# Kernel optimization log

Measured on AMD Instinct MI355X. Metric: run time of the kernel, lower is better.

Reference implementation:

```python
import jax, jax.numpy as jnp
import numpy as np

B, S, D, H = 2, 2048, 1024, 16
HD = D // H


def setup_inputs() -> dict:
    key = jax.random.key(0)
    ks = jax.random.split(key, 8)
    scale = 1.0 / np.sqrt(D)
    return {
        "x": jax.random.normal(ks[0], (B, S, D), dtype=jnp.float32),
        "y": jax.random.normal(ks[1], (B, S, D), dtype=jnp.float32),
        "gamma": jnp.ones((D,), jnp.float32),
        "beta": jnp.zeros((D,), jnp.float32),
        "in_proj_w": jax.random.uniform(ks[2], (3 * D, D), jnp.float32, -scale, scale),
        "in_proj_b": jnp.zeros((3 * D,), jnp.float32),
        "out_w": jax.random.uniform(ks[3], (D, D), jnp.float32, -scale, scale),
        "out_b": jnp.zeros((D,), jnp.float32),
    }


def _layer_norm(x, gamma, beta, eps=1e-5):
    mu = jnp.mean(x, axis=-1, keepdims=True)
    var = jnp.mean((x - mu) ** 2, axis=-1, keepdims=True)
    return (x - mu) * jax.lax.rsqrt(var + eps) * gamma + beta


def reference(x, y, gamma, beta, in_proj_w, in_proj_b, out_w, out_b):
    # Pre-LN (note: y is unused by the original forward; q=k=v=norm(x))
    xn = _layer_norm(x, gamma, beta)
    # combined QKV projection, PyTorch convention: xn @ W^T + b
    qkv = jnp.einsum("bsd,ed->bse", xn, in_proj_w) + in_proj_b  # (B,S,3D)
    q, k, v = jnp.split(qkv, 3, axis=-1)
    # (B,H,S,HD)
    q = q.reshape(B, S, H, HD).transpose(0, 2, 1, 3)
    k = k.reshape(B, S, H, HD).transpose(0, 2, 1, 3)
    v = v.reshape(B, S, H, HD).transpose(0, 2, 1, 3)
    scores = jnp.einsum("bhqd,bhkd->bhqk", q, k) / np.sqrt(HD)
    attn = jax.nn.softmax(scores, axis=-1)  # (B,H,S,S)
    ctx = jnp.einsum("bhqk,bhkd->bhqd", attn, v)
    ctx = ctx.transpose(0, 2, 1, 3).reshape(B, S, D)
    out = jnp.einsum("bsd,ed->bse", ctx, out_w) + out_b
    # dropout p=0.0 -> identity; residual
    out = out + x
    # average_attn_weights=True default in PyTorch
    attn_w = jnp.mean(attn, axis=1)  # (B,S,S)
    return out, attn_w
```

## Files before the change

### kernel.cpp

```cpp
#include <hip/hip_runtime.h>
#include <hip/hip_bf16.h>

#define Bb 2
#define Ss 2048
#define Dd 1024
#define Hh 16
#define HDd 64
#define Mm (Bb*Ss)
#define N3 (3*Dd)

typedef __attribute__((ext_vector_type(8))) __bf16 bf16x8;
typedef __attribute__((ext_vector_type(4))) float f32x4;
typedef __attribute__((ext_vector_type(16))) float f32x16;
typedef __attribute__((ext_vector_type(8))) short short8;

__device__ __forceinline__ unsigned short f2b(float f) {
  unsigned int u = __float_as_uint(f);
  return (unsigned short)((u + 0x7fffu + ((u >> 16) & 1u)) >> 16);
}

__device__ __forceinline__ f32x4 mfma16(bf16x8 a, bf16x8 b, f32x4 c) {
  return __builtin_amdgcn_mfma_f32_16x16x32_bf16(a, b, c, 0, 0, 0);
}
__device__ __forceinline__ f32x16 mfma32(bf16x8 a, bf16x8 b, f32x16 c) {
  return __builtin_amdgcn_mfma_f32_32x32x16_bf16(a, b, c, 0, 0, 0);
}
__device__ __forceinline__ unsigned cvtpk(float lo, float hi) {
  unsigned r; asm("v_cvt_pk_bf16_f32 %0, %1, %2" : "=v"(r) : "v"(lo), "v"(hi)); return r;
}
__device__ __forceinline__ float fexp2(float x) {
  float r; asm("v_exp_f32 %0, %1" : "=v"(r) : "v"(x)); return r;
}
__device__ __forceinline__ void gload16(const unsigned short* g, unsigned short* l) {
  __builtin_amdgcn_global_load_lds((const __attribute__((address_space(1))) void*)g,
                                   (__attribute__((address_space(3))) void*)l, 16, 0, 0);
}

__global__ __launch_bounds__(256) void prep_kernel(const float* __restrict__ x,
                                                   const float* __restrict__ gamma,
                                                   const float* __restrict__ beta,
                                                   unsigned short* __restrict__ xn,
                                                   const float* __restrict__ w_in,
                                                   unsigned short* __restrict__ wqkv,
                                                   const float* __restrict__ w_out,
                                                   unsigned short* __restrict__ wout) {
  const int bid = blockIdx.x, t = threadIdx.x;
  if (bid < Mm) {
    const float* xr = x + (size_t)bid * Dd;
    float4 v = ((const float4*)xr)[t];
    float s  = v.x + v.y + v.z + v.w;
    float ss = v.x*v.x + v.y*v.y + v.z*v.z + v.w*v.w;
    for (int m = 1; m < 64; m <<= 1) { s += __shfl_xor(s, m, 64); ss += __shfl_xor(ss, m, 64); }
    __shared__ float rs[4], rss[4];
    int w = t >> 6;
    if ((t & 63) == 0) { rs[w] = s; rss[w] = ss; }
    __syncthreads();
    s  = rs[0] + rs[1] + rs[2] + rs[3];
    ss = rss[0] + rss[1] + rss[2] + rss[3];
    float mu   = s * (1.0f / Dd);
    float var  = ss * (1.0f / Dd) - mu * mu;
    float rstd = rsqrtf(var + 1e-5f);
    float4 g  = ((const float4*)gamma)[t];
    float4 be = ((const float4*)beta)[t];
    ushort4 o;
    o.x = f2b((v.x - mu) * rstd * g.x + be.x);
    o.y = f2b((v.y - mu) * rstd * g.y + be.y);
    o.z = f2b((v.z - mu) * rstd * g.z + be.z);
    o.w = f2b((v.w - mu) * rstd * g.w + be.w);
    ((ushort4*)(xn + (size_t)bid * Dd))[t] = o;
  } else if (bid < Mm + 1024) {
    const int b2 = bid - Mm;
    for (int i = b2*256 + t; i < (N3*Dd)/4; i += 1024*256) {
      float4 v = ((const float4*)w_in)[i];
      ushort4 u; u.x = f2b(v.x); u.y = f2b(v.y); u.z = f2b(v.z); u.w = f2b(v.w);
      ((ushort4*)wqkv)[i] = u;
    }
  } else {
    const int b2 = bid - Mm - 1024;
    for (int i = b2*256 + t; i < (Dd*Dd)/4; i += 512*256) {
      float4 v = ((const float4*)w_out)[i];
      ushort4 u; u.x = f2b(v.x); u.y = f2b(v.y); u.z = f2b(v.z); u.w = f2b(v.w);
      ((ushort4*)wout)[i] = u;
    }
  }
}

__global__ __launch_bounds__(256) void qkv_gemm_kernel(
    const unsigned short* __restrict__ A, const unsigned short* __restrict__ Bw,
    const float* __restrict__ bias,
    unsigned short* __restrict__ qb, unsigned short* __restrict__ kb,
    unsigned short* __restrict__ vtb) {
  __shared__ __align__(16) unsigned short As[64][64];
  __shared__ __align__(16) unsigned short Bs[128][64];
  const int t = threadIdx.x, l = t & 63, w = t >> 6;
  const int wr = w >> 1, wc = w & 1;
  const int lin = blockIdx.x;
  const int swz = (lin & 7) * 192 + (lin >> 3);
  const int mb = (swz & 63) * 64, nb = (swz >> 6) * 128;
  const int sc8 = ((l & 7) ^ ((l >> 3) & 7)) * 8;
  f32x4 acc[2][4];
  for (int i = 0; i < 2; i++) for (int j = 0; j < 4; j++) acc[i][j] = f32x4{0.f,0.f,0.f,0.f};
  for (int kt = 0; kt < 1024; kt += 64) {
    __syncthreads();
#pragma unroll
    for (int j = 0; j < 2; ++j) {
      int rbase = w*16 + j*8;
      gload16(&A[(size_t)(mb + rbase + (l >> 3))*1024 + kt + sc8], &As[rbase][0]);
    }
#pragma unroll
    for (int j = 0; j < 4; ++j) {
      int rbase = w*32 + j*8;
      gload16(&Bw[(size_t)(nb + rbase + (l >> 3))*1024 + kt + sc8], &Bs[rbase][0]);
    }
    __syncthreads();
#pragma unroll
    for (int ks = 0; ks < 2; ++ks) {
      bf16x8 af[2], bfr[4];
      const int g = ks*4 + (l >> 4);
#pragma unroll
      for (int i = 0; i < 2; i++) {
        int row = wr*32 + i*16 + (l & 15);
        af[i] = *(const bf16x8*)&As[row][(g ^ (row & 7))*8];
      }
#pragma unroll
      for (int j = 0; j < 4; j++) {
        int row = wc*64 + j*16 + (l & 15);
        bfr[j] = *(const bf16x8*)&Bs[row][(g ^ (row & 7))*8];
      }
#pragma unroll
      for (int i = 0; i < 2; i++)
#pragma unroll
        for (int j = 0; j < 4; j++)
          acc[i][j] = mfma16(af[i], bfr[j], acc[i][j]);
    }
  }
  const int rbase = (l >> 4) * 4;
#pragma unroll
  for (int i = 0; i < 2; i++) {
#pragma unroll
    for (int j = 0; j < 4; j++) {
      int ncol = nb + wc*64 + j*16 + (l & 15);
      int which = ncol >> 10, d = ncol & 1023, h = d >> 6, hd = d & 63;
      float bv = bias[ncol];
      int mrow0 = mb + wr*32 + i*16 + rbase;
      int b = mrow0 >> 11, s0 = mrow0 & 2047;
      if (which == 2) {
        ushort4 u;
        u.x = f2b(acc[i][j][0] + bv); u.y = f2b(acc[i][j][1] + bv);
        u.z = f2b(acc[i][j][2] + bv); u.w = f2b(acc[i][j][3] + bv);
        *(ushort4*)&vtb[((size_t)(b*Hh + h)*HDd + hd)*Ss + s0] = u;
      } else {
        unsigned short* dst = (which == 0) ? qb : kb;
        float sc = (which == 0) ? 0.18033688f : 1.0f;
#pragma unroll
        for (int r = 0; r < 4; r++)
          dst[((size_t)(b*Hh + h)*Ss + s0 + r)*HDd + hd] = f2b((acc[i][j][r] + bv) * sc);
      }
    }
  }
}

__global__ __launch_bounds__(512) void ctx_kernel(const unsigned short* __restrict__ q,
                                                  const unsigned short* __restrict__ k,
                                                  const unsigned short* __restrict__ vt,
                                                  float* __restrict__ linv,
                                                  unsigned short* __restrict__ ctxb) {
  const int bh = blockIdx.x, qt = blockIdx.y;
  const int b = bh >> 4, h = bh & 15;
  const unsigned short* qp  = q  + (size_t)bh * Ss * HDd;
  const unsigned short* kp  = k  + (size_t)bh * Ss * HDd;
  const unsigned short* vtp = vt + (size_t)bh * HDd * Ss;
  const int t = threadIdx.x, l = t & 63, w = t >> 6;
  const int wq = w & 3, wk = w >> 2;
  const int l31 = l & 31, hi = l >> 5;
  __shared__ __align__(16) unsigned short Ks[2][2][64][64];
  __shared__ __align__(16) unsigned short Vs[2][2][64][64];
  __shared__ float ls[8][32];
  const int qbase = qt*128 + wq*32;
  const int sc8 = ((l & 7) ^ ((l >> 3) & 7)) * 8;
  const int kofs = wk * 1024;
  bf16x8 qfr[4];
#pragma unroll
  for (int c = 0; c < 4; ++c)
    qfr[c] = *(const bf16x8*)&qp[(size_t)(qbase + l31)*HDd + c*16 + hi*8];
#pragma unroll
  for (int j = 0; j < 2; ++j) {
    int rbase = wq*16 + j*8;
    int row = rbase + (l >> 3);
    gload16(&kp [(size_t)(kofs + row)*HDd + sc8], &Ks[wk][0][rbase][0]);
    gload16(&vtp[(size_t)row*Ss + kofs + sc8],    &Vs[wk][0][rbase][0]);
  }
  __syncthreads();

  f32x16 cacc[2];
#pragma unroll
  for (int dj = 0; dj < 2; ++dj)
#pragma unroll
    for (int r = 0; r < 16; ++r) cacc[dj][r] = 0.f;
  float lsum = 0.f;

  for (int it = 0; it < 16; ++it) {
    const int cur = it & 1;
    if (it < 15) {
      int kt = kofs + (it + 1) * 64;
#pragma unroll
      for (int j = 0; j < 2; ++j) {
        int rbase = wq*16 + j*8;
        int row = rbase + (l >> 3);
        gload16(&kp [(size_t)(kt + row)*HDd + sc8], &Ks[wk][cur^1][rbase][0]);
        gload16(&vtp[(size_t)row*Ss + kt + sc8],    &Vs[wk][cur^1][rbase][0]);
      }
    }
#pragma unroll
    for (int kj = 0; kj < 2; ++kj) {
      f32x16 sacc;
#pragma unroll
      for (int r = 0; r < 16; ++r) sacc[r] = 0.f;
      __builtin_amdgcn_s_setprio(1);
#pragma unroll
      for (int c = 0; c < 4; ++c) {
        int R = kj*32 + l31;
        int s = 2*c + hi;
        bf16x8 kf = *(const bf16x8*)&Ks[wk][cur][R][(s ^ (R & 7))*8];
        sacc = mfma32(kf, qfr[c], sacc);
      }
      __builtin_amdgcn_s_setprio(0);
      float p[16];
#pragma unroll
      for (int r = 0; r < 16; ++r) { p[r] = fexp2(sacc[r]); lsum += p[r]; }
      unsigned xa = cvtpk(p[0],p[1]),   xb = cvtpk(p[4],p[5]);
      unsigned ya = cvtpk(p[2],p[3]),   yb = cvtpk(p[6],p[7]);
      unsigned za = cvtpk(p[8],p[9]),   zb = cvtpk(p[12],p[13]);
      unsigned wa = cvtpk(p[10],p[11]), wb = cvtpk(p[14],p[15]);
      asm volatile("v_permlane32_swap_b32 %0, %1" : "+v"(xa), "+v"(xb));
      asm volatile("v_permlane32_swap_b32 %0, %1" : "+v"(ya), "+v"(yb));
      asm volatile("v_permlane32_swap_b32 %0, %1" : "+v"(za), "+v"(zb));
      asm volatile("v_permlane32_swap_b32 %0, %1" : "+v"(wa), "+v"(wb));
      union { unsigned u[4]; bf16x8 v; } f0, f1;
      f0.u[0]=xa; f0.u[1]=ya; f0.u[2]=xb; f0.u[3]=yb;
      f1.u[0]=za; f1.u[1]=wa; f1.u[2]=zb; f1.u[3]=wb;
      __builtin_amdgcn_s_setprio(1);
#pragma unroll
      for (int kc = 0; kc < 2; ++kc) {
        bf16x8 pa = kc ? f1.v : f0.v;
#pragma unroll
        for (int dj = 0; dj < 2; ++dj) {
          int Rv = dj*32 + l31;
          int s = 4*kj + 2*kc + hi;
          bf16x8 vb = *(const bf16x8*)&Vs[wk][cur][Rv][(s ^ (Rv & 7))*8];
          cacc[dj] = mfma32(pa, vb, cacc[dj]);
        }
      }
      __builtin_amdgcn_s_setprio(0);
    }
    __syncthreads();
  }
  lsum += __shfl_xor(lsum, 32, 64);
  if (l < 32) ls[w][l] = lsum;
  float* scr = (float*)&Ks[0][0][0][0];
  if (wk == 1) {
#pragma unroll
    for (int dj = 0; dj < 2; ++dj)
#pragma unroll
      for (int r = 0; r < 16; ++r)
        scr[((wq*2 + dj)*16 + r)*64 + l] = cacc[dj][r];
  }
  __syncthreads();
  if (wk == 0) {
#pragma unroll
    for (int dj = 0; dj < 2; ++dj)
#pragma unroll
      for (int r = 0; r < 16; ++r)
        cacc[dj][r] += scr[((wq*2 + dj)*16 + r)*64 + l];
    if (l < 32) {
      float li = 1.0f / (ls[w][l] + ls[w + 4][l]);
      ls[w][l] = li;
      linv[(size_t)bh*Ss + qbase + l] = li;
    }
    float li4[4][4];
#pragma unroll
    for (int g = 0; g < 4; ++g) {
      f32x4 v4 = *(const f32x4*)&ls[w][8*g + 4*hi];
#pragma unroll
      for (int j = 0; j < 4; ++j) li4[g][j] = v4[j];
    }
#pragma unroll
    for (int dj = 0; dj < 2; ++dj) {
      int d = h*64 + dj*32 + l31;
#pragma unroll
      for (int r = 0; r < 16; ++r) {
        int qq = qbase + (r & 3) + 8*(r >> 2) + 4*hi;
        ctxb[((size_t)b*Ss + qq)*Dd + d] = f2b(cacc[dj][r] * li4[r >> 2][r & 3]);
      }
    }
  }
}

__global__ __launch_bounds__(256) void attnw_out_kernel(
    const unsigned short* __restrict__ q, const unsigned short* __restrict__ k,
    const float* __restrict__ linv, float* __restrict__ attw,
    const unsigned short* __restrict__ ctxb, const unsigned short* __restrict__ wout,
    const float* __restrict__ bias, const float* __restrict__ x,
    float* __restrict__ outp) {
  __shared__ union __align__(16) {
    struct { unsigned short qbuf[128][64]; unsigned short kbuf[64][64]; } g;
    float ps[64][66];
    struct { unsigned short As[128][64]; unsigned short Bs[64][64]; } o;
  } L;
  const int t = threadIdx.x, l = t & 63, w = t >> 6;
  const int r3 = blockIdx.x % 3;
  if (r3 < 2) {
    const int lin = (blockIdx.x / 3) * 2 + r3;
    const int xcd = lin & 7, j0 = lin >> 3;
    const int ktile = (xcd & 3)*8 + (j0 & 7);
    const int qt    = (xcd >> 2)*8 + ((j0 >> 3) & 7);
    const int b     = j0 >> 6;
    const int l31 = l & 31, hi = l >> 5;
    const int qbase = qt*128 + w*32;
    const int qrow = qbase + l31;
    const int sc8 = ((l & 7) ^ ((l >> 3) & 7)) * 8;

    float psum[2][16];
#pragma unroll
    for (int kj = 0; kj < 2; ++kj)
#pragma unroll
      for (int r = 0; r < 16; ++r) psum[kj][r] = 0.f;

#pragma unroll 1
    for (int h = 0; h < 16; ++h) {
      __syncthreads();
      const unsigned short* qp = q + ((size_t)(b*Hh + h)*Ss + (size_t)qt*128)*HDd;
      const unsigned short* kp = k + ((size_t)(b*Hh + h)*Ss + (size_t)ktile*64)*HDd;
#pragma unroll
      for (int j = 0; j < 4; ++j) {
        int rbase = w*32 + j*8;
        gload16(&qp[(size_t)(rbase + (l >> 3))*HDd + sc8], &L.g.qbuf[rbase][0]);
      }
#pragma unroll
      for (int j = 0; j < 2; ++j) {
        int rbase = w*16 + j*8;
        gload16(&kp[(size_t)(rbase + (l >> 3))*HDd + sc8], &L.g.kbuf[rbase][0]);
      }
      float li = linv[(size_t)(b*Hh + h)*Ss + qrow];
      __syncthreads();
      bf16x8 qfr[4];
#pragma unroll
      for (int c = 0; c < 4; ++c) {
        int row = w*32 + l31;
        int s = 2*c + hi;
        qfr[c] = *(const bf16x8*)&L.g.qbuf[row][(s ^ (row & 7))*8];
      }
#pragma unroll
      for (int kj = 0; kj < 2; ++kj) {
        f32x16 sacc;
#pragma unroll
        for (int r = 0; r < 16; ++r) sacc[r] = 0.f;
        __builtin_amdgcn_s_setprio(1);
#pragma unroll
        for (int c = 0; c < 4; ++c) {
          int R = kj*32 + l31;
          int s = 2*c + hi;
          bf16x8 kf = *(const bf16x8*)&L.g.kbuf[R][(s ^ (R & 7))*8];
          sacc = mfma32(kf, qfr[c], sacc);
        }
        __builtin_amdgcn_s_setprio(0);
#pragma unroll
        for (int r = 0; r < 16; ++r) psum[kj][r] += fexp2(sacc[r]) * li;
      }
    }

#pragma unroll
    for (int p = 0; p < 2; ++p) {
      __syncthreads();
      if ((w >> 1) == p) {
#pragma unroll
        for (int kj = 0; kj < 2; ++kj)
#pragma unroll
          for (int r = 0; r < 16; ++r) {
            int krow = kj*32 + (r & 3) + 8*(r >> 2) + 4*hi;
            L.ps[(w & 1)*32 + l31][krow] = psum[kj][r] * (1.0f/16.0f);
          }
      }
      __syncthreads();
#pragma unroll
      for (int pass = 0; pass < 4; ++pass) {
        int row = pass*16 + (t >> 4), c4 = (t & 15) * 4;
        float4 v = *(const float4*)&L.ps[row][c4];
        *(float4*)&attw[((size_t)b*Ss + qt*128 + p*64 + row)*Ss + (size_t)ktile*64 + c4] = v;
      }
    }
  } else {
    const int ob = blockIdx.x / 3;
    const int wr = w >> 1, wc = w & 1;
    const int mb = (ob & 31) * 128, nb = (ob >> 5) * 64;
    const int sc8 = ((l & 7) ^ ((l >> 3) & 7)) * 8;
    f32x4 acc[4][2];
    for (int i = 0; i < 4; i++) for (int j = 0; j < 2; j++) acc[i][j] = f32x4{0.f,0.f,0.f,0.f};
    for (int kt = 0; kt < 1024; kt += 64) {
      __syncthreads();
#pragma unroll
      for (int j = 0; j < 4; ++j) {
        int rbase = w*32 + j*8;
        int row = rbase + (l >> 3);
        gload16(&ctxb[(size_t)(mb + row)*1024 + kt + sc8], &L.o.As[rbase][0]);
      }
#pragma unroll
      for (int j = 0; j < 2; ++j) {
        int rbase = w*16 + j*8;
        int row = rbase + (l >> 3);
        gload16(&wout[(size_t)(nb + row)*1024 + kt + sc8], &L.o.Bs[rbase][0]);
      }
      __syncthreads();
#pragma unroll
      for (int ks = 0; ks < 2; ++ks) {
        bf16x8 af[4], bfr[2];
        const int g = ks*4 + (l >> 4);
#pragma unroll
        for (int i = 0; i < 4; i++) {
          int row = wr*64 + i*16 + (l & 15);
          af[i] = *(const bf16x8*)&L.o.As[row][(g ^ (row & 7))*8];
        }
#pragma unroll
        for (int j = 0; j < 2; j++) {
          int row = wc*32 + j*16 + (l & 15);
          bfr[j] = *(const bf16x8*)&L.o.Bs[row][(g ^ (row & 7))*8];
        }
#pragma unroll
        for (int i = 0; i < 4; i++)
#pragma unroll
          for (int j = 0; j < 2; j++)
            acc[i][j] = mfma16(af[i], bfr[j], acc[i][j]);
      }
    }
    const int rbase = (l >> 4) * 4;
#pragma unroll
    for (int i = 0; i < 4; i++) {
#pragma unroll
      for (int j = 0; j < 2; j++) {
        int ncol = nb + wc*32 + j*16 + (l & 15);
        float bv = bias[ncol];
#pragma unroll
        for (int r = 0; r < 4; r++) {
          int mrow = mb + wr*64 + i*16 + rbase + r;
          size_t idx = (size_t)mrow * 1024 + ncol;
          outp[idx] = acc[i][j][r] + bv + x[idx];
        }
      }
    }
  }
}

extern "C" void kernel_launch(void* const* d_in, const int* in_sizes, int n_in,
                              void* d_out, int out_size, void* d_ws, size_t ws_size,
                              hipStream_t stream) {
  const float* x     = (const float*)d_in[0];
  const float* gamma = (const float*)d_in[2];
  const float* beta  = (const float*)d_in[3];
  const float* w_in  = (const float*)d_in[4];
  const float* b_in  = (const float*)d_in[5];
  const float* w_out = (const float*)d_in[6];
  const float* b_out = (const float*)d_in[7];
  float* outp = (float*)d_out;
  float* attw = outp + (size_t)Mm * Dd;

  char* ws = (char*)d_ws;
  unsigned short* xn   = (unsigned short*)(ws + 0);
  unsigned short* wqkv = (unsigned short*)(ws + 8388608);
  unsigned short* wout = (unsigned short*)(ws + 14680064);
  unsigned short* qb   = (unsigned short*)(ws + 16777216);
  unsigned short* kb   = (unsigned short*)(ws + 25165824);
  unsigned short* vtb  = (unsigned short*)(ws + 33554432);
  float*          linv = (float*)(ws + 41943040);
  unsigned short* ctxb = (unsigned short*)(ws + 42205184);

  prep_kernel<<<Mm + 1024 + 512, 256, 0, stream>>>(x, gamma, beta, xn, w_in, wqkv, w_out, wout);
  qkv_gemm_kernel<<<(Mm/64)*(N3/128), 256, 0, stream>>>(xn, wqkv, b_in, qb, kb, vtb);
  ctx_kernel<<<dim3(Bb*Hh, Ss/128), 512, 0, stream>>>(qb, kb, vtb, linv, ctxb);
  attnw_out_kernel<<<1536, 256, 0, stream>>>(qb, kb, linv, attw, ctxb, wout, b_out, x, outp);
}
```

Before: 137.3 us.

## Give every block both an attention-weight tile and a half-width output GEMM tile

Before, the fused kernel ran 1536 blocks, two of every three computing attention-weight tiles and the third computing a 128x64 output-projection tile. Now 1024 blocks each compute one attention-weight tile and one 128x32 output tile, with odd blocks doing the GEMM first and even blocks second. The aim is to even out per-block work, avoid a tail of mismatched block types, and mix the compute-bound and memory-bound phases across concurrent blocks. The narrower GEMM tile halves A-tile reuse and doubles how often ctx rows are loaded across blocks.

```diff
diff --git a/kernel.cpp b/kernel.cpp
--- a/kernel.cpp
+++ b/kernel.cpp
@@ -296,157 +296,166 @@
   }
 }
 
+union SharedU {
+  struct { unsigned short qbuf[128][64]; unsigned short kbuf[64][64]; } g;
+  float ps[64][66];
+  struct { unsigned short As[128][64]; unsigned short Bs[32][64]; } o;
+};
+
+__device__ __forceinline__ void attnw_part(SharedU& L,
+    const unsigned short* __restrict__ q, const unsigned short* __restrict__ k,
+    const float* __restrict__ linv, float* __restrict__ attw, int lin) {
+  const int t = threadIdx.x, l = t & 63, w = t >> 6;
+  const int xcd = lin & 7, j0 = lin >> 3;
+  const int ktile = (xcd & 3)*8 + (j0 & 7);
+  const int qt    = (xcd >> 2)*8 + ((j0 >> 3) & 7);
+  const int b     = j0 >> 6;
+  const int l31 = l & 31, hi = l >> 5;
+  const int qbase = qt*128 + w*32;
+  const int qrow = qbase + l31;
+  const int sc8 = ((l & 7) ^ ((l >> 3) & 7)) * 8;
+
+  float psum[2][16];
+#pragma unroll
+  for (int kj = 0; kj < 2; ++kj)
+#pragma unroll
+    for (int r = 0; r < 16; ++r) psum[kj][r] = 0.f;
+
+#pragma unroll 1
+  for (int h = 0; h < 16; ++h) {
+    __syncthreads();
+    const unsigned short* qp = q + ((size_t)(b*Hh + h)*Ss + (size_t)qt*128)*HDd;
+    const unsigned short* kp = k + ((size_t)(b*Hh + h)*Ss + (size_t)ktile*64)*HDd;
+#pragma unroll
+    for (int j = 0; j < 4; ++j) {
+      int rbase = w*32 + j*8;
+      gload16(&qp[(size_t)(rbase + (l >> 3))*HDd + sc8], &L.g.qbuf[rbase][0]);
+    }
+#pragma unroll
+    for (int j = 0; j < 2; ++j) {
+      int rbase = w*16 + j*8;
+      gload16(&kp[(size_t)(rbase + (l >> 3))*HDd + sc8], &L.g.kbuf[rbase][0]);
+    }
+    float li = linv[(size_t)(b*Hh + h)*Ss + qrow];
+    __syncthreads();
+    bf16x8 qfr[4];
+#pragma unroll
+    for (int c = 0; c < 4; ++c) {
+      int row = w*32 + l31;
+      int s = 2*c + hi;
+      qfr[c] = *(const bf16x8*)&L.g.qbuf[row][(s ^ (row & 7))*8];
+    }
+#pragma unroll
+    for (int kj = 0; kj < 2; ++kj) {
+      f32x16 sacc;
+#pragma unroll
+      for (int r = 0; r < 16; ++r) sacc[r] = 0.f;
+      __builtin_amdgcn_s_setprio(1);
+#pragma unroll
+      for (int c = 0; c < 4; ++c) {
+        int R = kj*32 + l31;
+        int s = 2*c + hi;
+        bf16x8 kf = *(const bf16x8*)&L.g.kbuf[R][(s ^ (R & 7))*8];
+        sacc = mfma32(kf, qfr[c], sacc);
+      }
+      __builtin_amdgcn_s_setprio(0);
+#pragma unroll
+      for (int r = 0; r < 16; ++r) psum[kj][r] += fexp2(sacc[r]) * li;
+    }
+  }
+
+#pragma unroll
+  for (int p = 0; p < 2; ++p) {
+    __syncthreads();
+    if ((w >> 1) == p) {
+#pragma unroll
+      for (int kj = 0; kj < 2; ++kj)
+#pragma unroll
+        for (int r = 0; r < 16; ++r) {
+          int krow = kj*32 + (r & 3) + 8*(r >> 2) + 4*hi;
+          L.ps[(w & 1)*32 + l31][krow] = psum[kj][r] * (1.0f/16.0f);
+        }
+    }
+    __syncthreads();
+#pragma unroll
+    for (int pass = 0; pass < 4; ++pass) {
+      int row = pass*16 + (t >> 4), c4 = (t & 15) * 4;
+      float4 v = *(const float4*)&L.ps[row][c4];
+      *(float4*)&attw[((size_t)b*Ss + qt*128 + p*64 + row)*Ss + (size_t)ktile*64 + c4] = v;
+    }
+  }
+}
+
+__device__ __forceinline__ void out_part(SharedU& L,
+    const unsigned short* __restrict__ ctxb, const unsigned short* __restrict__ wout,
+    const float* __restrict__ bias, const float* __restrict__ x,
+    float* __restrict__ outp, int ob) {
+  const int t = threadIdx.x, l = t & 63, w = t >> 6;
+  const int wr = w >> 1, wc = w & 1;
+  const int mb = (ob & 31) * 128, nb = (ob >> 5) * 32;
+  const int sc8 = ((l & 7) ^ ((l >> 3) & 7)) * 8;
+  f32x4 acc[4];
+  for (int i = 0; i < 4; i++) acc[i] = f32x4{0.f,0.f,0.f,0.f};
+  for (int kt = 0; kt < 1024; kt += 64) {
+    __syncthreads();
+#pragma unroll
+    for (int j = 0; j < 4; ++j) {
+      int rbase = w*32 + j*8;
+      int row = rbase + (l >> 3);
+      gload16(&ctxb[(size_t)(mb + row)*1024 + kt + sc8], &L.o.As[rbase][0]);
+    }
+    {
+      int rbase = w*8;
+      int row = rbase + (l >> 3);
+      gload16(&wout[(size_t)(nb + row)*1024 + kt + sc8], &L.o.Bs[rbase][0]);
+    }
+    __syncthreads();
+#pragma unroll
+    for (int ks = 0; ks < 2; ++ks) {
+      bf16x8 af[4], bfr;
+      const int g = ks*4 + (l >> 4);
+#pragma unroll
+      for (int i = 0; i < 4; i++) {
+        int row = wr*64 + i*16 + (l & 15);
+        af[i] = *(const bf16x8*)&L.o.As[row][(g ^ (row & 7))*8];
+      }
+      {
+        int row = wc*16 + (l & 15);
+        bfr = *(const bf16x8*)&L.o.Bs[row][(g ^ (row & 7))*8];
+      }
+#pragma unroll
+      for (int i = 0; i < 4; i++)
+        acc[i] = mfma16(af[i], bfr, acc[i]);
+    }
+  }
+  const int rbase = (l >> 4) * 4;
+#pragma unroll
+  for (int i = 0; i < 4; i++) {
+    int ncol = nb + wc*16 + (l & 15);
+    float bv = bias[ncol];
+#pragma unroll
+    for (int r = 0; r < 4; r++) {
+      int mrow = mb + wr*64 + i*16 + rbase + r;
+      size_t idx = (size_t)mrow * 1024 + ncol;
+      outp[idx] = acc[i][r] + bv + x[idx];
+    }
+  }
+}
+
 __global__ __launch_bounds__(256) void attnw_out_kernel(
     const unsigned short* __restrict__ q, const unsigned short* __restrict__ k,
     const float* __restrict__ linv, float* __restrict__ attw,
     const unsigned short* __restrict__ ctxb, const unsigned short* __restrict__ wout,
     const float* __restrict__ bias, const float* __restrict__ x,
     float* __restrict__ outp) {
-  __shared__ union __align__(16) {
-    struct { unsigned short qbuf[128][64]; unsigned short kbuf[64][64]; } g;
-    float ps[64][66];
-    struct { unsigned short As[128][64]; unsigned short Bs[64][64]; } o;
-  } L;
-  const int t = threadIdx.x, l = t & 63, w = t >> 6;
-  const int r3 = blockIdx.x % 3;
-  if (r3 < 2) {
-    const int lin = (blockIdx.x / 3) * 2 + r3;
-    const int xcd = lin & 7, j0 = lin >> 3;
-    const int ktile = (xcd & 3)*8 + (j0 & 7);
-    const int qt    = (xcd >> 2)*8 + ((j0 >> 3) & 7);
-    const int b     = j0 >> 6;
-    const int l31 = l & 31, hi = l >> 5;
-    const int qbase = qt*128 + w*32;
-    const int qrow = qbase + l31;
-    const int sc8 = ((l & 7) ^ ((l >> 3) & 7)) * 8;
-
-    float psum[2][16];
-#pragma unroll
-    for (int kj = 0; kj < 2; ++kj)
-#pragma unroll
-      for (int r = 0; r < 16; ++r) psum[kj][r] = 0.f;
-
-#pragma unroll 1
-    for (int h = 0; h < 16; ++h) {
-      __syncthreads();
-      const unsigned short* qp = q + ((size_t)(b*Hh + h)*Ss + (size_t)qt*128)*HDd;
-      const unsigned short* kp = k + ((size_t)(b*Hh + h)*Ss + (size_t)ktile*64)*HDd;
-#pragma unroll
-      for (int j = 0; j < 4; ++j) {
-        int rbase = w*32 + j*8;
-        gload16(&qp[(size_t)(rbase + (l >> 3))*HDd + sc8], &L.g.qbuf[rbase][0]);
-      }
-#pragma unroll
-      for (int j = 0; j < 2; ++j) {
-        int rbase = w*16 + j*8;
-        gload16(&kp[(size_t)(rbase + (l >> 3))*HDd + sc8], &L.g.kbuf[rbase][0]);
-      }
-      float li = linv[(size_t)(b*Hh + h)*Ss + qrow];
-      __syncthreads();
-      bf16x8 qfr[4];
-#pragma unroll
-      for (int c = 0; c < 4; ++c) {
-        int row = w*32 + l31;
-        int s = 2*c + hi;
-        qfr[c] = *(const bf16x8*)&L.g.qbuf[row][(s ^ (row & 7))*8];
-      }
-#pragma unroll
-      for (int kj = 0; kj < 2; ++kj) {
-        f32x16 sacc;
-#pragma unroll
-        for (int r = 0; r < 16; ++r) sacc[r] = 0.f;
-        __builtin_amdgcn_s_setprio(1);
-#pragma unroll
-        for (int c = 0; c < 4; ++c) {
-          int R = kj*32 + l31;
-          int s = 2*c + hi;
-          bf16x8 kf = *(const bf16x8*)&L.g.kbuf[R][(s ^ (R & 7))*8];
-          sacc = mfma32(kf, qfr[c], sacc);
-        }
-        __builtin_amdgcn_s_setprio(0);
-#pragma unroll
-        for (int r = 0; r < 16; ++r) psum[kj][r] += fexp2(sacc[r]) * li;
-      }
-    }
-
-#pragma unroll
-    for (int p = 0; p < 2; ++p) {
-      __syncthreads();
-      if ((w >> 1) == p) {
-#pragma unroll
-        for (int kj = 0; kj < 2; ++kj)
-#pragma unroll
-          for (int r = 0; r < 16; ++r) {
-            int krow = kj*32 + (r & 3) + 8*(r >> 2) + 4*hi;
-            L.ps[(w & 1)*32 + l31][krow] = psum[kj][r] * (1.0f/16.0f);
-          }
-      }
-      __syncthreads();
-#pragma unroll
-      for (int pass = 0; pass < 4; ++pass) {
-        int row = pass*16 + (t >> 4), c4 = (t & 15) * 4;
-        float4 v = *(const float4*)&L.ps[row][c4];
-        *(float4*)&attw[((size_t)b*Ss + qt*128 + p*64 + row)*Ss + (size_t)ktile*64 + c4] = v;
-      }
-    }
+  __shared__ SharedU L;
+  const int bid = blockIdx.x;
+  if (bid & 1) {
+    out_part(L, ctxb, wout, bias, x, outp, bid);
+    attnw_part(L, q, k, linv, attw, bid);
   } else {
-    const int ob = blockIdx.x / 3;
-    const int wr = w >> 1, wc = w & 1;
-    const int mb = (ob & 31) * 128, nb = (ob >> 5) * 64;
-    const int sc8 = ((l & 7) ^ ((l >> 3) & 7)) * 8;
-    f32x4 acc[4][2];
-    for (int i = 0; i < 4; i++) for (int j = 0; j < 2; j++) acc[i][j] = f32x4{0.f,0.f,0.f,0.f};
-    for (int kt = 0; kt < 1024; kt += 64) {
-      __syncthreads();
-#pragma unroll
-      for (int j = 0; j < 4; ++j) {
-        int rbase = w*32 + j*8;
-        int row = rbase + (l >> 3);
-        gload16(&ctxb[(size_t)(mb + row)*1024 + kt + sc8], &L.o.As[rbase][0]);
-      }
-#pragma unroll
-      for (int j = 0; j < 2; ++j) {
-        int rbase = w*16 + j*8;
-        int row = rbase + (l >> 3);
-        gload16(&wout[(size_t)(nb + row)*1024 + kt + sc8], &L.o.Bs[rbase][0]);
-      }
-      __syncthreads();
-#pragma unroll
-      for (int ks = 0; ks < 2; ++ks) {
-        bf16x8 af[4], bfr[2];
-        const int g = ks*4 + (l >> 4);
-#pragma unroll
-        for (int i = 0; i < 4; i++) {
-          int row = wr*64 + i*16 + (l & 15);
-          af[i] = *(const bf16x8*)&L.o.As[row][(g ^ (row & 7))*8];
-        }
-#pragma unroll
-        for (int j = 0; j < 2; j++) {
-          int row = wc*32 + j*16 + (l & 15);
-          bfr[j] = *(const bf16x8*)&L.o.Bs[row][(g ^ (row & 7))*8];
-        }
-#pragma unroll
-        for (int i = 0; i < 4; i++)
-#pragma unroll
-          for (int j = 0; j < 2; j++)
-            acc[i][j] = mfma16(af[i], bfr[j], acc[i][j]);
-      }
-    }
-    const int rbase = (l >> 4) * 4;
-#pragma unroll
-    for (int i = 0; i < 4; i++) {
-#pragma unroll
-      for (int j = 0; j < 2; j++) {
-        int ncol = nb + wc*32 + j*16 + (l & 15);
-        float bv = bias[ncol];
-#pragma unroll
-        for (int r = 0; r < 4; r++) {
-          int mrow = mb + wr*64 + i*16 + rbase + r;
-          size_t idx = (size_t)mrow * 1024 + ncol;
-          outp[idx] = acc[i][j][r] + bv + x[idx];
-        }
-      }
-    }
+    attnw_part(L, q, k, linv, attw, bid);
+    out_part(L, ctxb, wout, bias, x, outp, bid);
   }
 }
 
@@ -476,5 +485,5 @@
   prep_kernel<<<Mm + 1024 + 512, 256, 0, stream>>>(x, gamma, beta, xn, w_in, wqkv, w_out, wout);
   qkv_gemm_kernel<<<(Mm/64)*(N3/128), 256, 0, stream>>>(xn, wqkv, b_in, qb, kb, vtb);
   ctx_kernel<<<dim3(Bb*Hh, Ss/128), 512, 0, stream>>>(qb, kb, vtb, linv, ctxb);
-  attnw_out_kernel<<<1536, 256, 0, stream>>>(qb, kb, linv, attw, ctxb, wout, b_out, x, outp);
-}
+  attnw_out_kernel<<<1024, 256, 0, stream>>>(qb, kb, linv, attw, ctxb, wout, b_out, x, outp);
+}
```

New measurement: 188.8 us. +37.4%, slower.
